# Optimization experiments

Measured on AMD Instinct MI355X. Metric: run time of the kernel, lower is better.

The kernel has to match this reference:

```python
import jax, jax.numpy as jnp
import numpy as np
import math

HID = 1024      # opt.hidden_dim
NH = 8          # num_heads (hardcoded in module)
HD = HID // NH  # indiv_head_dim = 128
G = 16          # opt.group_num
GD = HID // G   # per-group dim = 64
FEAT = 1024     # opt.feature_dim
V, T = 8, 256   # videos x frames
E = 256         # number of events
L = 64          # max_att_len (clip window)
N = 384         # expanded event_num
WAVE = 10000.0


def setup_inputs() -> dict:
    rng = np.random.RandomState(0)
    key = jax.random.key(0)
    ks = jax.random.split(key, 12)

    feats = jax.random.normal(ks[0], (V * T, FEAT), dtype=jnp.float32)

    # ragged clip spans -> dense gather idx + mask (the Basic_Encoder loop)
    starts = rng.randint(0, V * T - L, size=(E,))
    clip_gather_idx = jnp.asarray(starts[:, None] + np.arange(L)[None, :], dtype=jnp.int32)
    lens = rng.randint(8, L + 1, size=(E,))
    clip_mask = jnp.asarray((np.arange(L)[None, :] < lens[:, None]).astype(np.float32))

    # event_seq_idx expansion: rows -> event ids, block-diagonal mask
    expand_idx = jnp.asarray(rng.randint(0, E, size=(N,)), dtype=jnp.int32)
    block_mask = np.zeros((N, N), dtype=np.float32)
    pos = 0
    while pos < N:
        b = min(int(rng.randint(8, 49)), N - pos)
        block_mask[pos:pos + b, pos:pos + b] = 1.0
        pos += b
    block_mask = jnp.asarray(block_mask)

    # normalized timestamps (start < end, in [0,1])
    s = rng.uniform(0.0, 0.8, size=(N, 1)).astype(np.float32)
    e = s + rng.uniform(0.02, 0.2, size=(N, 1)).astype(np.float32)
    bbox = jnp.asarray(np.concatenate([s, e], axis=1))

    sc = 1.0 / math.sqrt(HID)
    scd = 1.0 / math.sqrt(HD)
    Wpre = jax.random.normal(ks[1], (HID, FEAT), dtype=jnp.float32) * sc
    bpre = jnp.zeros((HID,), dtype=jnp.float32)
    Wq = jax.random.normal(ks[2], (NH, HD, HD), dtype=jnp.float32) * scd
    bq = jnp.zeros((NH, HD), dtype=jnp.float32)
    Wk = jax.random.normal(ks[3], (NH, HD, HD), dtype=jnp.float32) * scd
    bk = jnp.zeros((NH, HD), dtype=jnp.float32)
    Wv = jax.random.normal(ks[4], (NH, HD, HD), dtype=jnp.float32) * scd
    bv = jnp.zeros((NH, HD), dtype=jnp.float32)
    Wp1 = jax.random.normal(ks[5], (HID, HID), dtype=jnp.float32) * sc
    bp1 = jnp.zeros((HID,), dtype=jnp.float32)
    Wp2 = jax.random.normal(ks[6], (G, HID), dtype=jnp.float32) * sc
    bp2 = jnp.zeros((G,), dtype=jnp.float32)

    return dict(feats=feats, clip_gather_idx=clip_gather_idx, clip_mask=clip_mask,
                expand_idx=expand_idx, block_mask=block_mask, bbox=bbox,
                Wpre=Wpre, bpre=bpre, Wq=Wq, bq=bq, Wk=Wk, bk=bk, Wv=Wv, bv=bv,
                Wp1=Wp1, bp1=bp1, Wp2=Wp2, bp2=bp2)


def _sinusoid(x, feat_dim):
    # extract_position_embedding: x [..., P] -> [..., P*feat_dim/2*2] reshaped to feat_dim per row
    fr = jnp.arange(feat_dim // 4, dtype=x.dtype)
    dim_mat = WAVE ** (4.0 / feat_dim * fr)              # (feat_dim/4,)
    div = (100.0 * x)[..., None] / dim_mat               # (..., P, feat_dim/4)
    return jnp.concatenate([jnp.sin(div), jnp.cos(div)], axis=-1)


def reference(feats, clip_gather_idx, clip_mask, expand_idx, block_mask, bbox,
              Wpre, bpre, Wq, bq, Wk, bk, Wv, bv, Wp1, bp1, Wp2, bp2):
    # ---- clip-level pooling (Basic_Encoder.get_clip_level_feats + mean) ----
    clip_feats = feats[clip_gather_idx] * clip_mask[..., None]          # (E, L, FEAT)
    event = clip_feats.sum(1) / (clip_mask.sum(1, keepdims=True) + 1e-5)  # (E, FEAT)
    event = jax.nn.relu(event @ Wpre.T + bpre)                          # pre_map (dropout=eval)

    # ---- expand per event_seq_idx ----
    x = event[expand_idx]                                               # (N, HID)

    # ---- 8 per-head q/k/v maps, split into G groups ----
    xh = x.reshape(N, NH, HD)
    def proj(W, b):
        y = jnp.einsum('nhd,hed->nhe', xh, W) + b                       # (N, NH, HD)
        return y.reshape(N, G, GD).transpose(1, 0, 2)                   # (G, N, GD)
    q, k, v = proj(Wq, bq), proj(Wk, bk), proj(Wv, bv)
    scores = jnp.einsum('gnd,gmd->gnm', q, k) / math.sqrt(GD)           # (G, N, N)

    # ---- position branch: pairwise geometric relation bias ----
    start, end = bbox[:, 0:1], bbox[:, 1:2]                             # (N,1)
    center = 0.5 * (start + end)
    length = jnp.maximum(end - start, 0.1)
    dc = (center - center.T) / length
    dl = jnp.log(length.T / length)
    pm = jnp.stack([dc, dl], axis=2)                                    # (N, N, 2)
    emb = _sinusoid(pm, HID).reshape(N, N, HID)                         # (N, N, HID)
    pos = jax.nn.relu(emb @ Wp1.T + bp1)                                # pair_pos_fc1
    pos = jax.nn.relu(pos @ Wp2.T + bp2)                                # pair_pos_fc2 -> (N, N, G)
    pos_bias = jnp.log(jnp.clip(pos, 1e-6)).transpose(2, 0, 1)          # (G, N, N)

    scores = scores + pos_bias
    scores = jnp.where(block_mask[None] > 0, scores, -1e9)
    att = jax.nn.softmax(scores, axis=-1)                               # (G, N, N)
    out = jnp.einsum('gnm,gmd->gnd', att, v)                            # (G, N, GD)
    out = out.transpose(1, 0, 2).reshape(N, HID)

    # ---- per-event 100-dim temporal position embedding ----
    e100 = _sinusoid(bbox, 100).reshape(N, 100)

    return jnp.concatenate([x, out, e100], axis=-1)                     # (N, 2*HID + 100)
```

## Files before the change

### kernel.cpp

```cpp
#include <hip/hip_runtime.h>
#include <hip/hip_bf16.h>

typedef unsigned short u16;
typedef _Float16 h16;
typedef __attribute__((ext_vector_type(8))) h16 h8;
typedef __attribute__((ext_vector_type(4))) u16 us4;
typedef __attribute__((ext_vector_type(4))) float f4;

#define DEVFN __device__ __forceinline__

constexpr int kN = 384;
constexpr int kL = 64;
constexpr int kMaxP = kN * 48;
constexpr int kOutCols = 2148;
constexpr float kLoScale = 2048.f;
constexpr float kLoInv = 1.f / 2048.f;

union HU { h16 h; u16 u; };
DEVFN u16 f2h(float f) { HU c; c.h = (h16)f; return c.u; }
DEVFN float h2f(u16 b) { HU c; c.u = b; return (float)c.h; }

DEVFN f4 mfma16h(h8 a, h8 b, f4 c) {
  return __builtin_amdgcn_mfma_f32_16x16x32_f16(a, b, c, 0, 0, 0);
}

DEVFN h8 pack8h(float4 x0, float4 x1) {
  h8 a;
  a[0] = (h16)x0.x; a[1] = (h16)x0.y; a[2] = (h16)x0.z; a[3] = (h16)x0.w;
  a[4] = (h16)x1.x; a[5] = (h16)x1.y; a[6] = (h16)x1.z; a[7] = (h16)x1.w;
  return a;
}

DEVFN void fsincos(float ang, float& s, float& c) {
  float n = rintf(ang * 0.15915494309189535f);
  const float PI2_HI = 6.2831854820251465f;
  const float PI2_LO = -1.7484555e-07f;
  float r = fmaf(-n, PI2_HI, ang);
  r = fmaf(-n, PI2_LO, r);
  s = __sinf(r);
  c = __cosf(r);
}

__global__ __launch_bounds__(64) void k_ext(const float* __restrict__ bm,
                                            int* __restrict__ row_start,
                                            int* __restrict__ row_len) {
  int i = blockIdx.x, lane = threadIdx.x;
  int mn = kN, mx = -1;
  #pragma unroll
  for (int jb = 0; jb < kN; jb += 64) {
    float m = bm[(size_t)i * kN + jb + lane];
    if (m > 0.f) { mn = min(mn, jb + lane); mx = max(mx, jb + lane); }
  }
  #pragma unroll
  for (int off = 32; off > 0; off >>= 1) {
    mn = min(mn, __shfl_xor(mn, off));
    mx = max(mx, __shfl_xor(mx, off));
  }
  if (lane == 0) { row_start[i] = mn; row_len[i] = mx - mn + 1; }
}

__global__ __launch_bounds__(64) void k_scan(const int* __restrict__ row_len,
                                             int* __restrict__ row_off,
                                             int* __restrict__ Ptr) {
  int lane = threadIdx.x;
  int s[6], tot = 0;
  #pragma unroll
  for (int r = 0; r < 6; ++r) { s[r] = tot; tot += row_len[lane * 6 + r]; }
  int run = tot;
  #pragma unroll
  for (int off = 1; off < 64; off <<= 1) {
    int u = __shfl_up(run, off);
    if (lane >= off) run += u;
  }
  int excl = run - tot;
  #pragma unroll
  for (int r = 0; r < 6; ++r) row_off[lane * 6 + r] = excl + s[r];
  if (lane == 63) Ptr[0] = excl + tot;
}

__global__ __launch_bounds__(64) void k_fill(const int* __restrict__ row_start,
                                             const int* __restrict__ row_len,
                                             const int* __restrict__ row_off,
                                             int* __restrict__ pair_i,
                                             int* __restrict__ pair_j) {
  int i = blockIdx.x, lane = threadIdx.x;
  int s = row_start[i], len = row_len[i], off = row_off[i];
  if (lane < len) { pair_i[off + lane] = i; pair_j[off + lane] = s + lane; }
}

__global__ __launch_bounds__(256) void k_big(
    const float* __restrict__ Wp1, u16* __restrict__ W1H, u16* __restrict__ W1L,
    const float* __restrict__ Wp2, u16* __restrict__ W2H, u16* __restrict__ W2L,
    const float* __restrict__ Wpre, u16* __restrict__ WpreH,
    const float* __restrict__ Wq, u16* __restrict__ WqH,
    const float* __restrict__ Wk, u16* __restrict__ WkH,
    const float* __restrict__ Wv, u16* __restrict__ WvH,
    const float* __restrict__ feats, const int* __restrict__ gidx,
    const float* __restrict__ cmask, float* __restrict__ mean,
    float* __restrict__ bias_acc,
    const int* __restrict__ Ptr, const int* __restrict__ row_start,
    const int* __restrict__ row_off, const float* __restrict__ bbox,
    u16* __restrict__ ehi, u16* __restrict__ elo) {
  int bid = blockIdx.x, t = threadIdx.x;
  if (bid < 512) {
    const int nW1 = 1048576, nW2 = 16384, nPre = 1048576, nQ = 131072;
    const int tot = nW1 + nW2 + nPre + 3 * nQ;
    for (int i = bid * 256 + t; i < tot; i += 512 * 256) {
      if (i < nW1) {
        float x = Wp1[i]; u16 h = f2h(x);
        W1H[i] = h; W1L[i] = f2h((x - h2f(h)) * kLoScale);
      } else if (i < nW1 + nW2) {
        int j = i - nW1; float x = Wp2[j]; u16 h = f2h(x);
        W2H[j] = h; W2L[j] = f2h((x - h2f(h)) * kLoScale);
      } else if (i < nW1 + nW2 + nPre) {
        int j = i - nW1 - nW2; WpreH[j] = f2h(Wpre[j]);
      } else {
        int j = i - nW1 - nW2 - nPre;
        int a = j / nQ, r = j % nQ;
        const float* s = (a == 0) ? Wq : (a == 1) ? Wk : Wv;
        u16* d = (a == 0) ? WqH : (a == 1) ? WkH : WvH;
        d[r] = f2h(s[r]);
      }
    }
  } else if (bid < 768) {
    int e = bid - 512;
    float4 a = {0.f, 0.f, 0.f, 0.f};
    float ms = 0.f;
    for (int l = 0; l < kL; ++l) {
      float m = cmask[e * kL + l];
      ms += m;
      if (m > 0.f) {
        float4 v = *(const float4*)(feats + (size_t)gidx[e * kL + l] * 1024 + t * 4);
        a.x += v.x; a.y += v.y; a.z += v.z; a.w += v.w;
      }
    }
    float inv = 1.f / (ms + 1e-5f);
    float4 o = {a.x * inv, a.y * inv, a.z * inv, a.w * inv};
    *(float4*)(mean + (size_t)e * 1024 + t * 4) = o;
  } else if (bid < 816) {
    float4 z = {0.f, 0.f, 0.f, 0.f};
    for (int i4 = (bid - 768) * 256 + t; i4 < kMaxP * 16 / 4; i4 += 48 * 256)
      *(float4*)(bias_acc + (size_t)i4 * 4) = z;
  } else {
    int eb = bid - 816;
    int P = Ptr[0];
    int Pc = (P + 127) & ~127;
    if (eb * 2 >= Pc) return;
    __shared__ double As[16], Bs[16];
    __shared__ int roff[384], rstart[384];
    const double kCd = -13.287712379549449 / 256.0;
    if (t < 16) As[t] = exp2(kCd * (double)(t * 16));
    else if (t < 32) Bs[t - 16] = exp2(kCd * (double)(t - 16));
    for (int k = t; k < 384; k += 256) { roff[k] = row_off[k]; rstart[k] = row_start[k]; }
    __syncthreads();
    int p = eb * 2 + (t >> 7);
    int u = t & 127;
    int hseg = u >> 6;
    int f0 = (u & 63) * 4;
    size_t ob = (size_t)p * 1024 + hseg * 512 + f0;
    if (p >= P) {
      us4 z = {0, 0, 0, 0};
      *(us4*)(ehi + ob) = z; *(us4*)(ehi + ob + 256) = z;
      *(us4*)(elo + ob) = z; *(us4*)(elo + ob + 256) = z;
      return;
    }
    int lo = 0, hi = 383;
    while (lo < hi) { int md = (lo + hi + 1) >> 1; if (roff[md] <= p) lo = md; else hi = md - 1; }
    int pi = lo, pj = rstart[lo] + (p - roff[lo]);
    double s0 = bbox[pi * 2], e0 = bbox[pi * 2 + 1];
    double s1 = bbox[pj * 2], e1 = bbox[pj * 2 + 1];
    double li = fmax(e0 - s0, 0.1), lj = fmax(e1 - s1, 0.1);
    double x = hseg ? log(lj / li) : (0.5 * (s0 + e0) - 0.5 * (s1 + e1)) / li;
    double x100 = 100.0 * x;
    const double INV2PI = 0.15915494309189535;
    const double TWOPI  = 6.283185307179586;
    us4 sh_, sl_, ch_, cl_;
    #pragma unroll
    for (int j = 0; j < 4; ++j) {
      int f = f0 + j;
      double ang = x100 * (As[f >> 4] * Bs[f & 15]);
      double nn = rint(ang * INV2PI);
      float rf = (float)fma(-nn, TWOPI, ang);
      float sv = __sinf(rf), cv = __cosf(rf);
      u16 hs = f2h(sv); sh_[j] = hs; sl_[j] = f2h((sv - h2f(hs)) * kLoScale);
      u16 hc = f2h(cv); ch_[j] = hc; cl_[j] = f2h((cv - h2f(hc)) * kLoScale);
    }
    *(us4*)(ehi + ob) = sh_; *(us4*)(ehi + ob + 256) = ch_;
    *(us4*)(elo + ob) = sl_; *(us4*)(elo + ob + 256) = cl_;
  }
}

__global__ __launch_bounds__(256) void k_egemm(const float* __restrict__ mean,
                                               const u16* __restrict__ WpreH,
                                               const float* __restrict__ bpre,
                                               float* __restrict__ event) {
  int mt = blockIdx.x >> 4, nc = blockIdx.x & 15;
  int t = threadIdx.x;
  int w = t >> 6, lane = t & 63, lr = lane & 15, lg = lane >> 4;
  f4 acc = {};
  const float* arow = mean + (size_t)(mt * 16 + lr) * 1024;
  #pragma unroll
  for (int ks = 0; ks < 32; ++ks) {
    const float* ap = arow + ks * 32 + lg * 8;
    h8 a = pack8h(*(const float4*)ap, *(const float4*)(ap + 4));
    h8 b = *(const h8*)(WpreH + (size_t)(nc * 64 + w * 16 + lr) * 1024 + ks * 32 + lg * 8);
    acc = mfma16h(a, b, acc);
  }
  #pragma unroll
  for (int r = 0; r < 4; ++r) {
    int row = mt * 16 + lg * 4 + r, cn = nc * 64 + w * 16 + lr;
    event[(size_t)row * 1024 + cn] = fmaxf(acc[r] + bpre[cn], 0.f);
  }
}

__global__ __launch_bounds__(256, 2) void k_main(
    const int* __restrict__ Ptr, const u16* __restrict__ ehi, const u16* __restrict__ elo,
    const u16* __restrict__ W1h, const u16* __restrict__ W1l, const float* __restrict__ bias1,
    const u16* __restrict__ W2h, const u16* __restrict__ W2l, float* __restrict__ bias_acc,
    const float* __restrict__ event, const int* __restrict__ eidx,
    const u16* __restrict__ WqH, const float* __restrict__ bq,
    const u16* __restrict__ WkH, const float* __restrict__ bk,
    const u16* __restrict__ WvH, const float* __restrict__ bv,
    float* __restrict__ qb, float* __restrict__ kbuf, float* __restrict__ vbuf,
    int pos_on) {
  __shared__ u16 lds[2][4][4096];
  int bid = blockIdx.x, tid = threadIdx.x;
  if (bid < 1152) {
    if (!pos_on) return;
    int P = Ptr[0];
    int mb = bid % 144, nb = bid / 144;
    if (mb * 128 >= P) return;
    int w = tid >> 6, lane = tid & 63;
    int lr = lane & 15, lg = lane >> 4;
    int srow[2], scol[2];
    #pragma unroll
    for (int cc = 0; cc < 2; ++cc) {
      int c = w * 2 + cc;
      int d = c * 1024 + lane * 16;
      int b = d ^ (((((d >> 6) & 3)) ^ ((d >> 8) & 3)) << 4);
      srow[cc] = b >> 6;
      scol[cc] = b & 63;
    }
    const u16* planes[4] = {ehi, elo, W1h, W1l};
    int rb0 = mb * 128, rb1 = nb * 128;
    auto stage = [&](int buf, int k0) {
      #pragma unroll
      for (int t = 0; t < 4; ++t) {
        int rbase = (t < 2) ? rb0 : rb1;
        #pragma unroll
        for (int cc = 0; cc < 2; ++cc) {
          int c = w * 2 + cc;
          const char* src = (const char*)(planes[t] + (size_t)(rbase + srow[cc]) * 1024 + k0) + scol[cc];
          char* dst = (char*)&lds[buf][t][0] + c * 1024;
          __builtin_amdgcn_global_load_lds(
              (const __attribute__((address_space(1))) char*)src,
              (__attribute__((address_space(3))) char*)dst, 16, 0, 0);
        }
      }
    };
    stage(0, 0);
    f4 aH[4][4] = {}, aL[4][4] = {};
    int wm = (w >> 1) * 64, wn = (w & 1) * 64;
    int sl = (lg ^ (lr & 3) ^ ((lr >> 2) & 3)) << 4;
    __syncthreads();
    for (int kt = 0; kt < 32; ++kt) {
      int cur = kt & 1;
      if (kt < 31) stage(cur ^ 1, (kt + 1) * 32);
      h8 ah[4], al[4], bh[4], bl[4];
      #pragma unroll
      for (int mt = 0; mt < 4; ++mt) {
        int ad = (wm + mt * 16 + lr) * 64 + sl;
        ah[mt] = *(const h8*)((const char*)&lds[cur][0][0] + ad);
        al[mt] = *(const h8*)((const char*)&lds[cur][1][0] + ad);
      }
      #pragma unroll
      for (int nt = 0; nt < 4; ++nt) {
        int ad = (wn + nt * 16 + lr) * 64 + sl;
        bh[nt] = *(const h8*)((const char*)&lds[cur][2][0] + ad);
        bl[nt] = *(const h8*)((const char*)&lds[cur][3][0] + ad);
      }
      #pragma unroll
      for (int mt = 0; mt < 4; ++mt)
        #pragma unroll
        for (int nt = 0; nt < 4; ++nt) {
          aH[mt][nt] = mfma16h(ah[mt], bh[nt], aH[mt][nt]);
          aL[mt][nt] = mfma16h(al[mt], bh[nt], aL[mt][nt]);
          aL[mt][nt] = mfma16h(ah[mt], bl[nt], aL[mt][nt]);
        }
      __syncthreads();
    }
    float* zq = (float*)&lds[0][0][0] + w * 4096;
    #pragma unroll
    for (int mt = 0; mt < 4; ++mt)
      #pragma unroll
      for (int nt = 0; nt < 4; ++nt)
        #pragma unroll
        for (int r = 0; r < 4; ++r) {
          int pl = mt * 16 + lg * 4 + r;
          int nl = nt * 16 + lr;
          float z1 = aH[mt][nt][r] + aL[mt][nt][r] * kLoInv + bias1[nb * 128 + wn + nl];
          zq[pl * 64 + (nl ^ ((pl & 7) << 3))] = fmaxf(z1, 0.f);
        }
    __syncthreads();
    f4 c2h[4], c2l[4];
    #pragma unroll
    for (int i = 0; i < 4; ++i) { c2h[i] = f4{}; c2l[i] = f4{}; }
    #pragma unroll
    for (int mt2 = 0; mt2 < 4; ++mt2) {
      #pragma unroll
      for (int kc = 0; kc < 2; ++kc) {
        int pl = mt2 * 16 + lr;
        int n0 = kc * 32 + lg * 8;
        const float* rp = zq + pl * 64 + (n0 ^ ((pl & 7) << 3));
        float4 v0 = *(const float4*)rp;
        float4 v1 = *(const float4*)(rp + 4);
        h8 ah2, al2;
        #pragma unroll
        for (int j = 0; j < 4; ++j) {
          h16 h0 = (h16)v0[j]; ah2[j] = h0;     al2[j] = (h16)((v0[j] - (float)h0) * kLoScale);
          h16 h1 = (h16)v1[j]; ah2[4 + j] = h1; al2[4 + j] = (h16)((v1[j] - (float)h1) * kLoScale);
        }
        int ng = nb * 128 + wn + n0;
        h8 bh2 = *(const h8*)(W2h + lr * 1024 + ng);
        h8 bl2 = *(const h8*)(W2l + lr * 1024 + ng);
        c2h[mt2] = mfma16h(ah2, bh2, c2h[mt2]);
        c2l[mt2] = mfma16h(al2, bh2, c2l[mt2]);
        c2l[mt2] = mfma16h(ah2, bl2, c2l[mt2]);
      }
    }
    #pragma unroll
    for (int mt2 = 0; mt2 < 4; ++mt2)
      #pragma unroll
      for (int r = 0; r < 4; ++r) {
        int p = mb * 128 + wm + mt2 * 16 + lg * 4 + r;
        if (p < P)
          atomicAdd(&bias_acc[(size_t)p * 16 + lr], c2h[mt2][r] + c2l[mt2][r] * kLoInv);
      }
  } else {
    int b2 = bid - 1152;
    int z = b2 / 192, r2 = b2 % 192, mt = r2 >> 3, h = r2 & 7;
    int w = tid >> 6, lane = tid & 63, lr = lane & 15, lg = lane >> 4;
    const u16* W = (z == 0) ? WqH : (z == 1) ? WkH : WvH;
    const float* bias = (z == 0) ? bq : (z == 1) ? bk : bv;
    float* out = (z == 0) ? qb : (z == 1) ? kbuf : vbuf;
    int row = mt * 16 + lr;
    const float* arow = event + (size_t)eidx[row] * 1024 + h * 128;
    f4 acc[2] = {};
    #pragma unroll
    for (int ks = 0; ks < 4; ++ks) {
      const float* ap = arow + ks * 32 + lg * 8;
      h8 a = pack8h(*(const float4*)ap, *(const float4*)(ap + 4));
      #pragma unroll
      for (int n2 = 0; n2 < 2; ++n2) {
        int nt = w * 2 + n2;
        h8 b = *(const h8*)(W + h * 16384 + (nt * 16 + lr) * 128 + ks * 32 + lg * 8);
        acc[n2] = mfma16h(a, b, acc[n2]);
      }
    }
    #pragma unroll
    for (int n2 = 0; n2 < 2; ++n2)
      #pragma unroll
      for (int r = 0; r < 4; ++r) {
        int rn = mt * 16 + lg * 4 + r, e = (w * 2 + n2) * 16 + lr;
        out[(size_t)rn * 1024 + h * 128 + e] = acc[n2][r] + bias[h * 128 + e];
      }
  }
}

__global__ __launch_bounds__(64) void k_att(const float* __restrict__ q,
                                            const float* __restrict__ kk,
                                            const float* __restrict__ vv,
                                            const float* __restrict__ bias_acc,
                                            const float* __restrict__ bias2,
                                            const int* __restrict__ row_start,
                                            const int* __restrict__ row_len,
                                            const int* __restrict__ row_off,
                                            const float* __restrict__ event,
                                            const int* __restrict__ eidx,
                                            const float* __restrict__ bbox,
                                            float* __restrict__ dout) {
  int bid = blockIdx.x, lane = threadIdx.x;
  if (bid >= 6144) {
    int i = bid - 6144;
    const float* er = event + (size_t)eidx[i] * 1024;
    float* orow = dout + (size_t)i * kOutCols;
    #pragma unroll
    for (int it = 0; it < 4; ++it) {
      int c = lane * 4 + it * 256;
      *(float4*)(orow + c) = *(const float4*)(er + c);
    }
    for (int t = lane; t < 100; t += 64) {
      int qq = t / 25, f = t % 25;
      float x = bbox[i * 2 + (qq >> 1)];
      float ang = 100.f * x * exp2f((float)f * (-13.287712379549449f * 0.04f));
      float sv, cv;
      fsincos(ang, sv, cv);
      orow[2048 + t] = (qq & 1) ? cv : sv;
    }
    return;
  }
  int i = bid >> 4, g = bid & 15;
  int s = row_start[i], L = row_len[i], pb = row_off[i];
  __shared__ float qs[64];
  __shared__ float att[64];
  qs[lane] = q[(size_t)i * 1024 + g * 64 + lane];
  __syncthreads();
  bool valid = lane < L;
  const float* kr = kk + (size_t)(s + (valid ? lane : 0)) * 1024 + g * 64;
  float sc = 0.f;
  #pragma unroll
  for (int dt = 0; dt < 16; ++dt) {
    float4 kv = *(const float4*)(kr + dt * 4);
    sc += qs[dt * 4 + 0] * kv.x + qs[dt * 4 + 1] * kv.y +
          qs[dt * 4 + 2] * kv.z + qs[dt * 4 + 3] * kv.w;
  }
  int pidx = min(pb + lane, kMaxP - 1);
  float pbias = 0.f;
  if (valid) {
    float zs = bias_acc[(size_t)pidx * 16 + g] + bias2[g];
    pbias = logf(fmaxf(zs, 1e-6f));
  }
  sc = valid ? (sc * 0.125f + pbias) : -3.0e38f;
  float mx = sc;
  #pragma unroll
  for (int off = 32; off > 0; off >>= 1) mx = fmaxf(mx, __shfl_xor(mx, off));
  float pe = valid ? __expf(sc - mx) : 0.f;
  float sm = pe;
  #pragma unroll
  for (int off = 32; off > 0; off >>= 1) sm += __shfl_xor(sm, off);
  att[lane] = pe / sm;
  __syncthreads();
  float o = 0.f;
  const float* vb = vv + (size_t)s * 1024 + g * 64 + lane;
  for (int jl = 0; jl < L; ++jl) o += att[jl] * vb[(size_t)jl * 1024];
  dout[(size_t)i * kOutCols + 1024 + g * 64 + lane] = o;
}

__global__ __launch_bounds__(256) void k_pos(
    const int* __restrict__ Ptr, const int* __restrict__ pair_i,
    const int* __restrict__ pair_j, const float* __restrict__ bbox,
    const u16* __restrict__ W1h, const u16* __restrict__ W1l,
    const float* __restrict__ bias1,
    const u16* __restrict__ W2h, const u16* __restrict__ W2l,
    float* __restrict__ bias_acc) {
  int P = Ptr[0];
  int base0 = blockIdx.x * 64;
  if (base0 >= P) return;
  int w = threadIdx.x >> 6, l = threadIdx.x & 63;
  int lr = l & 15, lg = l >> 4;
  int base = base0 + w * 16;
  int p = base + lr;
  bool valid = p < P;
  int pi = valid ? pair_i[p] : 0;
  int pj = valid ? pair_j[p] : 0;
  double s0 = bbox[pi * 2], e0 = bbox[pi * 2 + 1];
  double s1 = bbox[pj * 2], e1 = bbox[pj * 2 + 1];
  double li = fmax(e0 - s0, 0.1), lj = fmax(e1 - s1, 0.1);
  double dcd = (0.5 * (s0 + e0) - 0.5 * (s1 + e1)) / li;
  double dld = log(lj / li);
  const double kCd = -13.287712379549449 / 256.0;
  double r1  = exp2(kCd);
  double r32 = exp2(kCd * 32.0);
  double pb0 = exp2(kCd * (double)(lg * 8));
  const double INV2PI = 0.15915494309189535;
  const double TWOPI  = 6.283185307179586;
  h8 eh[32], el[32];
  #pragma unroll
  for (int hx = 0; hx < 2; ++hx) {
    double x100 = 100.0 * (hx ? dld : dcd);
    double pch = pb0;
    #pragma unroll
    for (int ksl = 0; ksl < 8; ++ksl) {
      double pp = pch;
      #pragma unroll
      for (int j = 0; j < 8; ++j) {
        double ang = x100 * pp;
        double nn = rint(ang * INV2PI);
        float rf = (float)fma(-nn, TWOPI, ang);
        float sv = __sinf(rf), cv = __cosf(rf);
        h16 sh = (h16)sv, ch = (h16)cv;
        eh[hx * 16 + ksl][j] = sh;
        el[hx * 16 + ksl][j] = (h16)((sv - (float)sh) * kLoScale);
        eh[hx * 16 + 8 + ksl][j] = ch;
        el[hx * 16 + 8 + ksl][j] = (h16)((cv - (float)ch) * kLoScale);
        pp *= r1;
      }
      pch *= r32;
    }
  }
  __shared__ float p1f[4][16 * 64];
  char* myp1 = (char*)p1f[w];
  f4 acc2 = {}, acc2l = {};
  for (int nc = 0; nc < 16; ++nc) {
    f4 accH[4] = {}, accL[4] = {};
    #pragma unroll
    for (int ks = 0; ks < 32; ++ks) {
      #pragma unroll
      for (int nt = 0; nt < 4; ++nt) {
        size_t boff = (size_t)(nc * 64 + nt * 16 + lr) * 1024 + ks * 32 + lg * 8;
        h8 bh = *(const h8*)(W1h + boff);
        h8 bl = *(const h8*)(W1l + boff);
        accH[nt] = mfma16h(eh[ks], bh, accH[nt]);
        accL[nt] = mfma16h(el[ks], bh, accL[nt]);
        accL[nt] = mfma16h(eh[ks], bl, accL[nt]);
      }
    }
    __syncthreads();
    #pragma unroll
    for (int nt = 0; nt < 4; ++nt)
      #pragma unroll
      for (int r = 0; r < 4; ++r) {
        int m = lg * 4 + r, n = nt * 16 + lr;
        float z1 = accH[nt][r] + accL[nt][r] * kLoInv + bias1[nc * 64 + n];
        int byte = ((m * 64 + n) * 4) ^ ((m & 7) << 4);
        *(float*)(myp1 + byte) = fmaxf(z1, 0.f);
      }
    __syncthreads();
    #pragma unroll
    for (int hf = 0; hf < 2; ++hf) {
      int kb = hf * 32 + lg * 8;
      int b0 = ((lr * 64 + kb) * 4) ^ ((lr & 7) << 4);
      int b1 = ((lr * 64 + kb + 4) * 4) ^ ((lr & 7) << 4);
      float4 x0 = *(const float4*)(myp1 + b0);
      float4 x1 = *(const float4*)(myp1 + b1);
      h8 ah, al;
      #pragma unroll
      for (int j = 0; j < 4; ++j) {
        h16 h0 = (h16)x0[j];
        ah[j] = h0; al[j] = (h16)((x0[j] - (float)h0) * kLoScale);
        h16 h1 = (h16)x1[j];
        ah[4 + j] = h1; al[4 + j] = (h16)((x1[j] - (float)h1) * kLoScale);
      }
      h8 bh = *(const h8*)(W2h + lr * 1024 + nc * 64 + kb);
      h8 bl = *(const h8*)(W2l + lr * 1024 + nc * 64 + kb);
      acc2  = mfma16h(ah, bh, acc2);
      acc2l = mfma16h(al, bh, acc2l);
      acc2l = mfma16h(ah, bl, acc2l);
    }
  }
  #pragma unroll
  for (int r = 0; r < 4; ++r) {
    int m = lg * 4 + r;
    int pp = base + m;
    if (pp < P)
      bias_acc[(size_t)pp * 16 + lr] = acc2[r] + acc2l[r] * kLoInv;
  }
}

extern "C" void kernel_launch(void* const* d_in, const int* in_sizes, int n_in,
                              void* d_out, int out_size, void* d_ws, size_t ws_size,
                              hipStream_t stream) {
  const float* feats = (const float*)d_in[0];
  const int*   gidx  = (const int*)d_in[1];
  const float* cmask = (const float*)d_in[2];
  const int*   eidx  = (const int*)d_in[3];
  const float* bmask = (const float*)d_in[4];
  const float* bbox  = (const float*)d_in[5];
  const float* Wpre  = (const float*)d_in[6];
  const float* bpre  = (const float*)d_in[7];
  const float* Wq    = (const float*)d_in[8];
  const float* bq    = (const float*)d_in[9];
  const float* Wk    = (const float*)d_in[10];
  const float* bk    = (const float*)d_in[11];
  const float* Wv    = (const float*)d_in[12];
  const float* bv    = (const float*)d_in[13];
  const float* Wp1   = (const float*)d_in[14];
  const float* bp1   = (const float*)d_in[15];
  const float* Wp2   = (const float*)d_in[16];
  const float* bp2   = (const float*)d_in[17];

  char* ws = (char*)d_ws;
  size_t off = 0;
  auto alloc = [&](size_t bytes) {
    char* r = ws + off;
    off += (bytes + 255) & ~(size_t)255;
    return r;
  };
  u16* W1H   = (u16*)alloc((size_t)1048576 * 2);
  u16* W1L   = (u16*)alloc((size_t)1048576 * 2);
  u16* W2H   = (u16*)alloc((size_t)16384 * 2);
  u16* W2L   = (u16*)alloc((size_t)16384 * 2);
  u16* WpreH = (u16*)alloc((size_t)1048576 * 2);
  u16* WqH   = (u16*)alloc((size_t)131072 * 2);
  u16* WkH   = (u16*)alloc((size_t)131072 * 2);
  u16* WvH   = (u16*)alloc((size_t)131072 * 2);
  float* mean  = (float*)alloc((size_t)256 * 1024 * 4);
  float* event = (float*)alloc((size_t)256 * 1024 * 4);
  float* qb    = (float*)alloc((size_t)384 * 1024 * 4);
  float* kb    = (float*)alloc((size_t)384 * 1024 * 4);
  float* vb    = (float*)alloc((size_t)384 * 1024 * 4);
  int* row_start = (int*)alloc(kN * 4);
  int* row_len   = (int*)alloc(kN * 4);
  int* row_off   = (int*)alloc(kN * 4);
  int* Ptr       = (int*)alloc(256);
  int* pair_i    = (int*)alloc((size_t)kMaxP * 4);
  int* pair_j    = (int*)alloc((size_t)kMaxP * 4);
  float* bias_acc = (float*)alloc((size_t)kMaxP * 16 * 4);
  u16* ehi      = (u16*)alloc((size_t)kMaxP * 1024 * 2);
  u16* elo      = (u16*)alloc((size_t)kMaxP * 1024 * 2);
  bool fast = (off <= ws_size);

  k_ext<<<kN, 64, 0, stream>>>(bmask, row_start, row_len);
  k_scan<<<1, 64, 0, stream>>>(row_len, row_off, Ptr);
  k_big<<<10032, 256, 0, stream>>>(Wp1, W1H, W1L, Wp2, W2H, W2L, Wpre, WpreH,
                                   Wq, WqH, Wk, WkH, Wv, WvH,
                                   feats, gidx, cmask, mean, bias_acc,
                                   Ptr, row_start, row_off, bbox, ehi, elo);
  k_egemm<<<256, 256, 0, stream>>>(mean, WpreH, bpre, event);

  if (fast) {
    k_main<<<1728, 256, 0, stream>>>(Ptr, ehi, elo, W1H, W1L, bp1, W2H, W2L, bias_acc,
                                     event, eidx, WqH, bq, WkH, bk, WvH, bv,
                                     qb, kb, vb, 1);
  } else {
    k_fill<<<kN, 64, 0, stream>>>(row_start, row_len, row_off, pair_i, pair_j);
    k_pos<<<kMaxP / 64, 256, 0, stream>>>(Ptr, pair_i, pair_j, bbox, W1H, W1L, bp1,
                                          W2H, W2L, bias_acc);
    k_main<<<1728, 256, 0, stream>>>(Ptr, ehi, elo, W1H, W1L, bp1, W2H, W2L, bias_acc,
                                     event, eidx, WqH, bq, WkH, bk, WvH, bv,
                                     qb, kb, vb, 0);
  }
  k_att<<<6528, 64, 0, stream>>>(qb, kb, vb, bias_acc, bp2, row_start, row_len, row_off,
                                 event, eidx, bbox, (float*)d_out);
}
```

Measured before the change: 156.0 us.

## Fold event GEMM into k_big and merge mask-extent, clip-mean and zeroing kernel

Moves the clip-mean and bias-accumulator zeroing out of k_big into a new combined pre-kernel alongside the mask row-extent pass. The event projection GEMM now runs inside k_big and reads fp32 Wpre directly, converting it to fp16 on the fly, so the separate fp16 Wpre conversion pass, its buffer and the k_egemm launch are dropped. The attention output loop is split into four independent accumulators for more memory-level parallelism. This removes one launch and a 1M-element conversion pass, at the cost of each GEMM block reading fp32 weights at twice the bytes.

```diff
diff --git a/kernel.cpp b/kernel.cpp
--- a/kernel.cpp
+++ b/kernel.cpp
@@ -41,22 +41,47 @@
   c = __cosf(r);
 }
 
-__global__ __launch_bounds__(64) void k_ext(const float* __restrict__ bm,
-                                            int* __restrict__ row_start,
-                                            int* __restrict__ row_len) {
-  int i = blockIdx.x, lane = threadIdx.x;
-  int mn = kN, mx = -1;
-  #pragma unroll
-  for (int jb = 0; jb < kN; jb += 64) {
-    float m = bm[(size_t)i * kN + jb + lane];
-    if (m > 0.f) { mn = min(mn, jb + lane); mx = max(mx, jb + lane); }
-  }
-  #pragma unroll
-  for (int off = 32; off > 0; off >>= 1) {
-    mn = min(mn, __shfl_xor(mn, off));
-    mx = max(mx, __shfl_xor(mx, off));
-  }
-  if (lane == 0) { row_start[i] = mn; row_len[i] = mx - mn + 1; }
+__global__ __launch_bounds__(256) void k_pre(
+    const float* __restrict__ bm, int* __restrict__ row_start, int* __restrict__ row_len,
+    const float* __restrict__ feats, const int* __restrict__ gidx,
+    const float* __restrict__ cmask, float* __restrict__ mean,
+    float* __restrict__ bias_acc) {
+  int bid = blockIdx.x, t = threadIdx.x;
+  if (bid < 96) {
+    int w = t >> 6, lane = t & 63;
+    int i = bid * 4 + w;
+    int mn = kN, mx = -1;
+    #pragma unroll
+    for (int jb = 0; jb < kN; jb += 64) {
+      float m = bm[(size_t)i * kN + jb + lane];
+      if (m > 0.f) { mn = min(mn, jb + lane); mx = max(mx, jb + lane); }
+    }
+    #pragma unroll
+    for (int off = 32; off > 0; off >>= 1) {
+      mn = min(mn, __shfl_xor(mn, off));
+      mx = max(mx, __shfl_xor(mx, off));
+    }
+    if (lane == 0) { row_start[i] = mn; row_len[i] = mx - mn + 1; }
+  } else if (bid < 352) {
+    int e = bid - 96;
+    float4 a = {0.f, 0.f, 0.f, 0.f};
+    float ms = 0.f;
+    for (int l = 0; l < kL; ++l) {
+      float m = cmask[e * kL + l];
+      ms += m;
+      if (m > 0.f) {
+        float4 v = *(const float4*)(feats + (size_t)gidx[e * kL + l] * 1024 + t * 4);
+        a.x += v.x; a.y += v.y; a.z += v.z; a.w += v.w;
+      }
+    }
+    float inv = 1.f / (ms + 1e-5f);
+    float4 o = {a.x * inv, a.y * inv, a.z * inv, a.w * inv};
+    *(float4*)(mean + (size_t)e * 1024 + t * 4) = o;
+  } else {
+    float4 z = {0.f, 0.f, 0.f, 0.f};
+    for (int i4 = (bid - 352) * 256 + t; i4 < kMaxP * 16 / 4; i4 += 48 * 256)
+      *(float4*)(bias_acc + (size_t)i4 * 4) = z;
+  }
 }
 
 __global__ __launch_bounds__(64) void k_scan(const int* __restrict__ row_len,
@@ -91,58 +116,54 @@
 __global__ __launch_bounds__(256) void k_big(
     const float* __restrict__ Wp1, u16* __restrict__ W1H, u16* __restrict__ W1L,
     const float* __restrict__ Wp2, u16* __restrict__ W2H, u16* __restrict__ W2L,
-    const float* __restrict__ Wpre, u16* __restrict__ WpreH,
     const float* __restrict__ Wq, u16* __restrict__ WqH,
     const float* __restrict__ Wk, u16* __restrict__ WkH,
     const float* __restrict__ Wv, u16* __restrict__ WvH,
-    const float* __restrict__ feats, const int* __restrict__ gidx,
-    const float* __restrict__ cmask, float* __restrict__ mean,
-    float* __restrict__ bias_acc,
+    const float* __restrict__ mean, const float* __restrict__ Wpre,
+    const float* __restrict__ bpre, float* __restrict__ event,
     const int* __restrict__ Ptr, const int* __restrict__ row_start,
     const int* __restrict__ row_off, const float* __restrict__ bbox,
     u16* __restrict__ ehi, u16* __restrict__ elo) {
   int bid = blockIdx.x, t = threadIdx.x;
-  if (bid < 512) {
-    const int nW1 = 1048576, nW2 = 16384, nPre = 1048576, nQ = 131072;
-    const int tot = nW1 + nW2 + nPre + 3 * nQ;
-    for (int i = bid * 256 + t; i < tot; i += 512 * 256) {
+  if (bid < 256) {
+    int mt = bid >> 4, nc = bid & 15;
+    int w = t >> 6, lane = t & 63, lr = lane & 15, lg = lane >> 4;
+    f4 acc = {};
+    const float* arow = mean + (size_t)(mt * 16 + lr) * 1024;
+    const float* brow = Wpre + (size_t)(nc * 64 + w * 16 + lr) * 1024;
+    #pragma unroll
+    for (int ks = 0; ks < 32; ++ks) {
+      const float* ap = arow + ks * 32 + lg * 8;
+      const float* bp = brow + ks * 32 + lg * 8;
+      h8 a = pack8h(*(const float4*)ap, *(const float4*)(ap + 4));
+      h8 b = pack8h(*(const float4*)bp, *(const float4*)(bp + 4));
+      acc = mfma16h(a, b, acc);
+    }
+    #pragma unroll
+    for (int r = 0; r < 4; ++r) {
+      int row = mt * 16 + lg * 4 + r, cn = nc * 64 + w * 16 + lr;
+      event[(size_t)row * 1024 + cn] = fmaxf(acc[r] + bpre[cn], 0.f);
+    }
+  } else if (bid < 768) {
+    const int nW1 = 1048576, nW2 = 16384, nQ = 131072;
+    const int tot = nW1 + nW2 + 3 * nQ;
+    for (int i = (bid - 256) * 256 + t; i < tot; i += 512 * 256) {
       if (i < nW1) {
         float x = Wp1[i]; u16 h = f2h(x);
         W1H[i] = h; W1L[i] = f2h((x - h2f(h)) * kLoScale);
       } else if (i < nW1 + nW2) {
         int j = i - nW1; float x = Wp2[j]; u16 h = f2h(x);
         W2H[j] = h; W2L[j] = f2h((x - h2f(h)) * kLoScale);
-      } else if (i < nW1 + nW2 + nPre) {
-        int j = i - nW1 - nW2; WpreH[j] = f2h(Wpre[j]);
       } else {
-        int j = i - nW1 - nW2 - nPre;
+        int j = i - nW1 - nW2;
         int a = j / nQ, r = j % nQ;
         const float* s = (a == 0) ? Wq : (a == 1) ? Wk : Wv;
         u16* d = (a == 0) ? WqH : (a == 1) ? WkH : WvH;
         d[r] = f2h(s[r]);
       }
     }
-  } else if (bid < 768) {
-    int e = bid - 512;
-    float4 a = {0.f, 0.f, 0.f, 0.f};
-    float ms = 0.f;
-    for (int l = 0; l < kL; ++l) {
-      float m = cmask[e * kL + l];
-      ms += m;
-      if (m > 0.f) {
-        float4 v = *(const float4*)(feats + (size_t)gidx[e * kL + l] * 1024 + t * 4);
-        a.x += v.x; a.y += v.y; a.z += v.z; a.w += v.w;
-      }
-    }
-    float inv = 1.f / (ms + 1e-5f);
-    float4 o = {a.x * inv, a.y * inv, a.z * inv, a.w * inv};
-    *(float4*)(mean + (size_t)e * 1024 + t * 4) = o;
-  } else if (bid < 816) {
-    float4 z = {0.f, 0.f, 0.f, 0.f};
-    for (int i4 = (bid - 768) * 256 + t; i4 < kMaxP * 16 / 4; i4 += 48 * 256)
-      *(float4*)(bias_acc + (size_t)i4 * 4) = z;
   } else {
-    int eb = bid - 816;
+    int eb = bid - 768;
     int P = Ptr[0];
     int Pc = (P + 127) & ~127;
     if (eb * 2 >= Pc) return;
@@ -190,29 +211,6 @@
   }
 }
 
-__global__ __launch_bounds__(256) void k_egemm(const float* __restrict__ mean,
-                                               const u16* __restrict__ WpreH,
-                                               const float* __restrict__ bpre,
-                                               float* __restrict__ event) {
-  int mt = blockIdx.x >> 4, nc = blockIdx.x & 15;
-  int t = threadIdx.x;
-  int w = t >> 6, lane = t & 63, lr = lane & 15, lg = lane >> 4;
-  f4 acc = {};
-  const float* arow = mean + (size_t)(mt * 16 + lr) * 1024;
-  #pragma unroll
-  for (int ks = 0; ks < 32; ++ks) {
-    const float* ap = arow + ks * 32 + lg * 8;
-    h8 a = pack8h(*(const float4*)ap, *(const float4*)(ap + 4));
-    h8 b = *(const h8*)(WpreH + (size_t)(nc * 64 + w * 16 + lr) * 1024 + ks * 32 + lg * 8);
-    acc = mfma16h(a, b, acc);
-  }
-  #pragma unroll
-  for (int r = 0; r < 4; ++r) {
-    int row = mt * 16 + lg * 4 + r, cn = nc * 64 + w * 16 + lr;
-    event[(size_t)row * 1024 + cn] = fmaxf(acc[r] + bpre[cn], 0.f);
-  }
-}
-
 __global__ __launch_bounds__(256, 2) void k_main(
     const int* __restrict__ Ptr, const u16* __restrict__ ehi, const u16* __restrict__ elo,
     const u16* __restrict__ W1h, const u16* __restrict__ W1l, const float* __restrict__ bias1,
@@ -430,10 +428,17 @@
   for (int off = 32; off > 0; off >>= 1) sm += __shfl_xor(sm, off);
   att[lane] = pe / sm;
   __syncthreads();
-  float o = 0.f;
+  float o0 = 0.f, o1 = 0.f, o2 = 0.f, o3 = 0.f;
   const float* vb = vv + (size_t)s * 1024 + g * 64 + lane;
-  for (int jl = 0; jl < L; ++jl) o += att[jl] * vb[(size_t)jl * 1024];
-  dout[(size_t)i * kOutCols + 1024 + g * 64 + lane] = o;
+  int jl = 0;
+  for (; jl + 3 < L; jl += 4) {
+    o0 += att[jl]     * vb[(size_t)jl * 1024];
+    o1 += att[jl + 1] * vb[(size_t)(jl + 1) * 1024];
+    o2 += att[jl + 2] * vb[(size_t)(jl + 2) * 1024];
+    o3 += att[jl + 3] * vb[(size_t)(jl + 3) * 1024];
+  }
+  for (; jl < L; ++jl) o0 += att[jl] * vb[(size_t)jl * 1024];
+  dout[(size_t)i * kOutCols + 1024 + g * 64 + lane] = (o0 + o1) + (o2 + o3);
 }
 
 __global__ __launch_bounds__(256) void k_pos(
@@ -580,7 +585,6 @@
   u16* W1L   = (u16*)alloc((size_t)1048576 * 2);
   u16* W2H   = (u16*)alloc((size_t)16384 * 2);
   u16* W2L   = (u16*)alloc((size_t)16384 * 2);
-  u16* WpreH = (u16*)alloc((size_t)1048576 * 2);
   u16* WqH   = (u16*)alloc((size_t)131072 * 2);
   u16* WkH   = (u16*)alloc((size_t)131072 * 2);
   u16* WvH   = (u16*)alloc((size_t)131072 * 2);
@@ -600,13 +604,13 @@
   u16* elo      = (u16*)alloc((size_t)kMaxP * 1024 * 2);
   bool fast = (off <= ws_size);
 
-  k_ext<<<kN, 64, 0, stream>>>(bmask, row_start, row_len);
+  k_pre<<<400, 256, 0, stream>>>(bmask, row_start, row_len,
+                                 feats, gidx, cmask, mean, bias_acc);
   k_scan<<<1, 64, 0, stream>>>(row_len, row_off, Ptr);
-  k_big<<<10032, 256, 0, stream>>>(Wp1, W1H, W1L, Wp2, W2H, W2L, Wpre, WpreH,
-                                   Wq, WqH, Wk, WkH, Wv, WvH,
-                                   feats, gidx, cmask, mean, bias_acc,
-                                   Ptr, row_start, row_off, bbox, ehi, elo);
-  k_egemm<<<256, 256, 0, stream>>>(mean, WpreH, bpre, event);
+  k_big<<<9984, 256, 0, stream>>>(Wp1, W1H, W1L, Wp2, W2H, W2L,
+                                  Wq, WqH, Wk, WkH, Wv, WvH,
+                                  mean, Wpre, bpre, event,
+                                  Ptr, row_start, row_off, bbox, ehi, elo);
 
   if (fast) {
     k_main<<<1728, 256, 0, stream>>>(Ptr, ehi, elo, W1H, W1L, bp1, W2H, W2L, bias_acc,
```

Result: no change. 153.9 us, median of 2 (-1.4%).
